# Performance work log

Hardware: AMD Instinct MI355X
Metric: run time of the kernel (lower is better)

## Reference

```python
import jax, jax.numpy as jnp
import numpy as np

N_EMBD = 768
N_EXP = 8
DIM_HIDDEN = int(N_EMBD * 4 * 2 / 3)  # 2048
B = 8
CAP = 1024


def setup_inputs() -> dict:
    key = jax.random.key(0)
    k1, k2, k3 = jax.random.split(key, 3)
    std_fc = N_EXP ** (-0.5)  # matches torch init: dim = c_fc.shape[0] = n_exp
    x = jax.random.normal(k1, (B, N_EXP, CAP, N_EMBD), dtype=jnp.float32)
    c_fc = jax.random.uniform(k2, (N_EXP, N_EMBD, 2 * DIM_HIDDEN), dtype=jnp.float32,
                              minval=-std_fc, maxval=std_fc)
    c_proj = jax.random.uniform(k3, (N_EXP, DIM_HIDDEN, N_EMBD), dtype=jnp.float32,
                                minval=-std_fc, maxval=std_fc)
    gamma = jnp.ones((N_EMBD,), dtype=jnp.float32)       # RMSNorm gamma
    mult_bias = jnp.ones((DIM_HIDDEN,), dtype=jnp.float32)  # GEGLU mult_bias
    return {"x": x, "c_fc": c_fc, "c_proj": c_proj, "gamma": gamma, "mult_bias": mult_bias}


def _moe_forward(x, c_fc, c_proj, gamma, mult_bias):
    # x: [b, e, n, d] -> [e, b, n, d]
    h = jnp.transpose(x, (1, 0, 2, 3))
    # RMSNorm (prenorm): F.normalize(x, dim=-1) * gamma * sqrt(d)
    scale = N_EMBD ** 0.5
    l2 = jnp.sqrt(jnp.sum(h * h, axis=-1, keepdims=True))
    h = h / jnp.maximum(l2, 1e-12) * gamma * scale
    # per-expert grouped GEMM: [e,b,n,d] @ [e,d,2h] -> [e,b,n,2h]
    u = jnp.einsum('ebnd,edh->ebnh', h, c_fc)
    # GEGLU: first half is value, second half is gate
    v, gate = u[..., :DIM_HIDDEN], u[..., DIM_HIDDEN:]
    g = jax.nn.gelu(gate, approximate=False) * v * mult_bias
    # project back: [e,b,n,h] @ [e,h,d] -> [e,b,n,d]
    out = jnp.einsum('ebnh,ehd->ebnd', g, c_proj)
    # back to [b, e, n, d]; dropout is identity (p=0.0)
    return jnp.transpose(out, (1, 0, 2, 3))


def reference(x, c_fc, c_proj, gamma, mult_bias):
    return _moe_forward(x, c_fc, c_proj, gamma, mult_bias)
```

## Files before the change

### kernel.cpp

```cpp
#include <hip/hip_runtime.h>
#include <math.h>

#define N_EMBD 768
#define N_EXP  8
#define DIMH   2048
#define CAPN   1024
#define M_TOT  8192

typedef __bf16 bf16x8 __attribute__((ext_vector_type(8)));
typedef float  f32x4  __attribute__((ext_vector_type(4)));

__device__ __forceinline__ unsigned short f2bf(float f) {
    unsigned int u = __float_as_uint(f);
    unsigned int r = (u + 0x7fffu + ((u >> 16) & 1u)) >> 16;
    return (unsigned short)r;
}

__device__ __forceinline__ void gload16(const void* g, void* l) {
    __builtin_amdgcn_global_load_lds(
        (const __attribute__((address_space(1))) unsigned int*)g,
        (__attribute__((address_space(3))) unsigned int*)l, 16, 0, 0);
}

__global__ __launch_bounds__(256) void norm_convert_kernel(
        const float* __restrict__ x, const float* __restrict__ gamma,
        unsigned short* __restrict__ h) {
    int r = blockIdx.x;
    int e = r >> 13, m = r & 8191;
    int b = m >> 10, nc = m & 1023;
    const float* row = x + (size_t)((b * N_EXP + e) * CAPN + nc) * N_EMBD;
    unsigned short* orow = h + (size_t)(e * M_TOT + m) * N_EMBD;
    int t = threadIdx.x;

    float v0 = row[t], v1 = row[t + 256], v2 = row[t + 512];
    float acc = v0 * v0 + v1 * v1 + v2 * v2;
#pragma unroll
    for (int off = 32; off >= 1; off >>= 1) acc += __shfl_down(acc, off, 64);
    __shared__ float part[4];
    if ((t & 63) == 0) part[t >> 6] = acc;
    __syncthreads();
    float tot = part[0] + part[1] + part[2] + part[3];
    float s = 27.712812921102035f / fmaxf(sqrtf(tot), 1e-12f);

    orow[t]       = f2bf(v0 * s * gamma[t]);
    orow[t + 256] = f2bf(v1 * s * gamma[t + 256]);
    orow[t + 512] = f2bf(v2 * s * gamma[t + 512]);
}

__global__ __launch_bounds__(256) void transpose_convert_kernel(
        const float* __restrict__ in, unsigned short* __restrict__ out, int R, int C) {
    __shared__ float tile[32][33];
    int c0 = blockIdx.x * 32, r0 = blockIdx.y * 32;
    const float* ip = in + (size_t)blockIdx.z * R * C;
    unsigned short* op = out + (size_t)blockIdx.z * R * C;
    int tx = threadIdx.x & 31, ty = threadIdx.x >> 5;
#pragma unroll
    for (int i = 0; i < 4; ++i)
        tile[ty + 8 * i][tx] = ip[(size_t)(r0 + ty + 8 * i) * C + c0 + tx];
    __syncthreads();
#pragma unroll
    for (int i = 0; i < 4; ++i)
        op[(size_t)(c0 + ty + 8 * i) * R + r0 + tx] = f2bf(tile[tx][ty + 8 * i]);
}

#define SBB  __builtin_amdgcn_s_barrier(); \
             asm volatile("s_waitcnt lgkmcnt(0)" ::: "memory"); \
             __builtin_amdgcn_sched_barrier(0); \
             __builtin_amdgcn_s_setprio(1)
#define SBE  __builtin_amdgcn_s_setprio(0); __builtin_amdgcn_s_barrier()
#define VMW(N) do { asm volatile("s_waitcnt vmcnt(" #N ")" ::: "memory"); \
             __builtin_amdgcn_sched_barrier(0); } while (0)

#define STG2(PSRC, RS, KT, DOFF) do { \
    gload16((PSRC) + (size_t)sr * (RS) + (size_t)(KT) * 64 + scs, lds + (DOFF) + ldst); \
    gload16((PSRC) + (size_t)(sr + 64) * (RS) + (size_t)(KT) * 64 + scs, lds + (DOFF) + ldst + 4096); \
  } while (0)

#define RDF(V) (*(const bf16x8*)(lds + (V)))

#define RDA4(AF, DB, IB) do { \
    _Pragma("unroll") for (int i_ = 0; i_ < 4; ++i_) { \
      AF[i_][0] = RDF((DB)*32768 + aB + ((IB) + i_)*1024 + sl0); \
      AF[i_][1] = RDF((DB)*32768 + aB + ((IB) + i_)*1024 + sl1); } \
  } while (0)

#define RDB2(BF, DB, BASE) do { \
    _Pragma("unroll") for (int j_ = 0; j_ < 2; ++j_) { \
      BF[j_][0] = RDF((DB)*32768 + (BASE) + j_*1024 + sl0); \
      BF[j_][1] = RDF((DB)*32768 + (BASE) + j_*1024 + sl1); } \
  } while (0)

#define QUAD(ACC, MS, NB, AF, BF) do { \
    _Pragma("unroll") for (int i_ = 0; i_ < 4; ++i_) \
    _Pragma("unroll") for (int j_ = 0; j_ < 2; ++j_) { \
      ACC[(MS)*4 + i_][(NB) + j_] = __builtin_amdgcn_mfma_f32_16x16x32_bf16( \
          AF[i_][0], BF[j_][0], ACC[(MS)*4 + i_][(NB) + j_], 0, 0, 0); \
      ACC[(MS)*4 + i_][(NB) + j_] = __builtin_amdgcn_mfma_f32_16x16x32_bf16( \
          AF[i_][1], BF[j_][1], ACC[(MS)*4 + i_][(NB) + j_], 0, 0, 0); } \
  } while (0)

__global__ __launch_bounds__(512, 2) void gemm1_kernel(
        const unsigned short* __restrict__ hb,
        const unsigned short* __restrict__ fT,
        const float* __restrict__ mbias,
        unsigned short* __restrict__ gb,
        int e0) {
    __shared__ __align__(16) unsigned short lds[65536];
    const int t = threadIdx.x;
    const int e = e0 + blockIdx.z;
    const int m0 = blockIdx.x * 256;
    const int n0 = blockIdx.y * 128;
    const unsigned short* pA  = hb + ((size_t)e * M_TOT + m0) * N_EMBD;
    const unsigned short* pBv = fT + ((size_t)e * 2 * DIMH + n0) * N_EMBD;
    const unsigned short* pBg = pBv + (size_t)DIMH * N_EMBD;
    unsigned short* pG = gb + (size_t)blockIdx.z * M_TOT * DIMH;

    const int sr   = t >> 3;
    const int scs  = ((t & 7) ^ (sr & 7)) * 8;
    const int ldst = t * 8;
    const int lane = t & 63, lo = lane & 15, quad = lane >> 4;
    const int w = t >> 6, wm = w & 1, wn = w >> 1;
    const int sl0 = ((quad    ) ^ (lo & 7)) * 8;
    const int sl1 = ((quad + 4) ^ (lo & 7)) * 8;
    const int aB  = wm * 8192 + lo * 64;
    const int bvB = 16384 + (wn * 32 + lo) * 64;
    const int bgB = 24576 + (wn * 32 + lo) * 64;

#define STA1(D, H, KT)  STG2(pA + (size_t)(H) * 128 * N_EMBD, N_EMBD, KT, (D)*32768 + (H)*8192)
#define STBV1(D, KT)    STG2(pBv, N_EMBD, KT, (D)*32768 + 16384)
#define STBG1(D, KT)    STG2(pBg, N_EMBD, KT, (D)*32768 + 24576)

    f32x4 accv[8][2], accg[8][2];
#pragma unroll
    for (int i = 0; i < 8; ++i)
#pragma unroll
        for (int j = 0; j < 2; ++j) { accv[i][j] = (f32x4)0.f; accg[i][j] = (f32x4)0.f; }
    bf16x8 a0[4][2], a1[4][2], bv[2][2], bg[2][2];

    STA1(0, 0, 0); STA1(0, 1, 0); STBV1(0, 0); STBG1(0, 0); STA1(1, 0, 1);
    VMW(2);
    __builtin_amdgcn_s_barrier();

    for (int it = 0; it < 6; ++it) {
        const int kb = 2 * it + 1, kc = kb + 1, kd = kb + 2;
        const bool more = (it < 5);
        RDA4(a0, 0, 0); RDB2(bv, 0, bvB);
        STA1(1, 1, kb);
        SBB; QUAD(accv, 0, 0, a0, bv); SBE;
        RDA4(a1, 0, 4);
        STBV1(1, kb);
        SBB; QUAD(accv, 1, 0, a1, bv); SBE;
        RDB2(bg, 0, bgB);
        STBG1(1, kb);
        SBB; QUAD(accg, 1, 0, a1, bg); SBE;
        if (more) { STA1(0, 0, kc); VMW(2); } else { VMW(0); }
        SBB; QUAD(accg, 0, 0, a0, bg); SBE;
        RDA4(a0, 1, 0); RDB2(bv, 1, bvB);
        if (more) STA1(0, 1, kc);
        SBB; QUAD(accv, 0, 0, a0, bv); SBE;
        RDA4(a1, 1, 4);
        if (more) STBV1(0, kc);
        SBB; QUAD(accv, 1, 0, a1, bv); SBE;
        RDB2(bg, 1, bgB);
        if (more) STBG1(0, kc);
        SBB; QUAD(accg, 1, 0, a1, bg); SBE;
        if (more) { STA1(1, 0, kd); VMW(2); } else { VMW(0); }
        SBB; QUAD(accg, 0, 0, a0, bg); SBE;
    }

#pragma unroll
    for (int i = 0; i < 8; ++i) {
        const int mb = m0 + wm * 128 + i * 16 + quad * 4;
#pragma unroll
        for (int j = 0; j < 2; ++j) {
            const int n = n0 + wn * 32 + j * 16 + lo;
            const float mbv = mbias[n];
#pragma unroll
            for (int r = 0; r < 4; ++r) {
                float gt = accg[i][j][r];
                float ge = 0.5f * gt * (1.0f + erff(gt * 0.70710678118654752f));
                pG[(size_t)(mb + r) * DIMH + n] = f2bf(ge * accv[i][j][r] * mbv);
            }
        }
    }
#undef STA1
#undef STBV1
#undef STBG1
}

__global__ __launch_bounds__(512, 2) void gemm2_kernel(
        const unsigned short* __restrict__ gb,
        const unsigned short* __restrict__ pT,
        float* __restrict__ out, int e0) {
    __shared__ __align__(16) unsigned short lds[65536];
    const int t = threadIdx.x;
    const int e = e0 + blockIdx.z;
    const int m0 = blockIdx.x * 256;
    const int n0 = blockIdx.y * 256;
    const unsigned short* pA = gb + (size_t)blockIdx.z * M_TOT * DIMH + (size_t)m0 * DIMH;
    const unsigned short* pB = pT + ((size_t)e * N_EMBD + n0) * DIMH;

    const int sr   = t >> 3;
    const int scs  = ((t & 7) ^ (sr & 7)) * 8;
    const int ldst = t * 8;
    const int lane = t & 63, lo = lane & 15, quad = lane >> 4;
    const int w = t >> 6, wm = w & 1, wn = w >> 1;
    const int sl0 = ((quad    ) ^ (lo & 7)) * 8;
    const int sl1 = ((quad + 4) ^ (lo & 7)) * 8;
    const int aB  = wm * 8192 + lo * 64;
    const int bB  = 16384 + (wn >> 1) * 8192 + ((wn & 1) * 64 + lo) * 64;

#define STA2(D, H, KT)  STG2(pA + (size_t)(H) * 128 * DIMH, DIMH, KT, (D)*32768 + (H)*8192)
#define STB2(D, H, KT)  STG2(pB + (size_t)(H) * 128 * DIMH, DIMH, KT, (D)*32768 + 16384 + (H)*8192)

    f32x4 acc[8][4];
#pragma unroll
    for (int i = 0; i < 8; ++i)
#pragma unroll
        for (int j = 0; j < 4; ++j) acc[i][j] = (f32x4)0.f;
    bf16x8 a0[4][2], a1[4][2], bb[2][2];

    STA2(0, 0, 0); STA2(0, 1, 0); STB2(0, 0, 0); STB2(0, 1, 0); STA2(1, 0, 1);
    VMW(2);
    __builtin_amdgcn_s_barrier();

    for (int it = 0; it < 16; ++it) {
        const int kb = 2 * it + 1, kc = kb + 1, kd = kb + 2;
        const bool more = (it < 15);
        RDA4(a0, 0, 0); RDB2(bb, 0, bB);
        STA2(1, 1, kb);
        SBB; QUAD(acc, 0, 0, a0, bb); SBE;
        RDA4(a1, 0, 4);
        STB2(1, 0, kb);
        SBB; QUAD(acc, 1, 0, a1, bb); SBE;
        RDB2(bb, 0, bB + 2048);
        STB2(1, 1, kb);
        SBB; QUAD(acc, 1, 2, a1, bb); SBE;
        if (more) { STA2(0, 0, kc); VMW(2); } else { VMW(0); }
        SBB; QUAD(acc, 0, 2, a0, bb); SBE;
        RDA4(a0, 1, 0); RDB2(bb, 1, bB);
        if (more) STA2(0, 1, kc);
        SBB; QUAD(acc, 0, 0, a0, bb); SBE;
        RDA4(a1, 1, 4);
        if (more) STB2(0, 0, kc);
        SBB; QUAD(acc, 1, 0, a1, bb); SBE;
        RDB2(bb, 1, bB + 2048);
        if (more) STB2(0, 1, kc);
        SBB; QUAD(acc, 1, 2, a1, bb); SBE;
        if (more) { STA2(1, 0, kd); VMW(2); } else { VMW(0); }
        SBB; QUAD(acc, 0, 2, a0, bb); SBE;
    }

#pragma unroll
    for (int i = 0; i < 8; ++i) {
        const int mb = m0 + wm * 128 + i * 16 + quad * 4;
#pragma unroll
        for (int r = 0; r < 4; ++r) {
            const int m = mb + r;
            const int b = m >> 10, nc = m & 1023;
            float* orow = out + (size_t)((b * N_EXP + e) * CAPN + nc) * N_EMBD;
#pragma unroll
            for (int j = 0; j < 4; ++j)
                orow[n0 + wn * 64 + j * 16 + lo] = acc[i][j][r];
        }
    }
#undef STA2
#undef STB2
}

extern "C" void kernel_launch(void* const* d_in, const int* in_sizes, int n_in,
                              void* d_out, int out_size, void* d_ws, size_t ws_size,
                              hipStream_t stream) {
    const float* x     = (const float*)d_in[0];
    const float* cfc   = (const float*)d_in[1];
    const float* cproj = (const float*)d_in[2];
    const float* gamma = (const float*)d_in[3];
    const float* mbias = (const float*)d_in[4];
    float* out = (float*)d_out;

    unsigned short* h      = (unsigned short*)d_ws;
    unsigned short* cfcT   = h + 50331648ull;
    unsigned short* cprojT = cfcT + 25165824ull;
    unsigned short* gbuf   = cprojT + 12582912ull;
    const size_t need_batched = 444596224ull;

    norm_convert_kernel<<<dim3(N_EXP * M_TOT), dim3(256), 0, stream>>>(x, gamma, h);
    transpose_convert_kernel<<<dim3(2 * DIMH / 32, N_EMBD / 32, N_EXP), dim3(256), 0, stream>>>(
        cfc, cfcT, N_EMBD, 2 * DIMH);
    transpose_convert_kernel<<<dim3(N_EMBD / 32, DIMH / 32, N_EXP), dim3(256), 0, stream>>>(
        cproj, cprojT, DIMH, N_EMBD);

    if (ws_size >= need_batched) {
        gemm1_kernel<<<dim3(M_TOT / 256, DIMH / 128, N_EXP), dim3(512), 0, stream>>>(
            h, cfcT, mbias, gbuf, 0);
        gemm2_kernel<<<dim3(M_TOT / 256, N_EMBD / 256, N_EXP), dim3(512), 0, stream>>>(
            gbuf, cprojT, out, 0);
    } else {
        for (int e = 0; e < N_EXP; ++e) {
            gemm1_kernel<<<dim3(M_TOT / 256, DIMH / 128, 1), dim3(512), 0, stream>>>(
                h, cfcT, mbias, gbuf, e);
            gemm2_kernel<<<dim3(M_TOT / 256, N_EMBD / 256, 1), dim3(512), 0, stream>>>(
                gbuf, cprojT, out, e);
        }
    }
}
```

Before: 1.263 ms.

## Restructure GEMM prefetch schedule, vectorize norm kernel, use polynomial erf GELU

The norm kernel now processes one row per wavefront with float4 loads, u16x4 stores and xor-shuffle reduction, which removes the shared-memory barrier and cuts the block count. Both GEMM kernels change their global-to-LDS prefetch: each half-iteration issues the whole next K tile at once, then waits with vmcnt(0) before the last MFMA quad, replacing the staggered issue with partial vmcnt waits. The GELU epilogue swaps erff for the Abramowitz-Stegun polynomial using a fast reciprocal and __expf. In exchange the GELU is slightly less accurate, and the coarser full waits may expose more load latency.

```diff
diff --git a/kernel.cpp b/kernel.cpp
--- a/kernel.cpp
+++ b/kernel.cpp
@@ -9,6 +9,7 @@
 
 typedef __bf16 bf16x8 __attribute__((ext_vector_type(8)));
 typedef float  f32x4  __attribute__((ext_vector_type(4)));
+typedef unsigned short u16x4 __attribute__((ext_vector_type(4)));
 
 __device__ __forceinline__ unsigned short f2bf(float f) {
     unsigned int u = __float_as_uint(f);
@@ -22,29 +23,47 @@
         (__attribute__((address_space(3))) unsigned int*)l, 16, 0, 0);
 }
 
+__device__ __forceinline__ float gelu_exact(float x) {
+    float ax = fabsf(x);
+    float z  = ax * 0.70710678118654752f;
+    float t  = __builtin_amdgcn_rcpf(fmaf(0.3275911f, z, 1.0f));
+    float p  = fmaf(t, 1.061405429f, -1.453152027f);
+    p = fmaf(p, t, 1.421413741f);
+    p = fmaf(p, t, -0.284496736f);
+    p = fmaf(p, t, 0.254829592f);
+    p = p * t;
+    float ez = __expf(-z * z);
+    float erfz = fmaf(-p, ez, 1.0f);
+    return 0.5f * fmaf(ax, erfz, x);
+}
+
 __global__ __launch_bounds__(256) void norm_convert_kernel(
         const float* __restrict__ x, const float* __restrict__ gamma,
         unsigned short* __restrict__ h) {
-    int r = blockIdx.x;
+    int r = (blockIdx.x << 2) | (threadIdx.x >> 6);
+    int lane = threadIdx.x & 63;
     int e = r >> 13, m = r & 8191;
     int b = m >> 10, nc = m & 1023;
-    const float* row = x + (size_t)((b * N_EXP + e) * CAPN + nc) * N_EMBD;
-    unsigned short* orow = h + (size_t)(e * M_TOT + m) * N_EMBD;
-    int t = threadIdx.x;
-
-    float v0 = row[t], v1 = row[t + 256], v2 = row[t + 512];
-    float acc = v0 * v0 + v1 * v1 + v2 * v2;
-#pragma unroll
-    for (int off = 32; off >= 1; off >>= 1) acc += __shfl_down(acc, off, 64);
-    __shared__ float part[4];
-    if ((t & 63) == 0) part[t >> 6] = acc;
-    __syncthreads();
-    float tot = part[0] + part[1] + part[2] + part[3];
-    float s = 27.712812921102035f / fmaxf(sqrtf(tot), 1e-12f);
-
-    orow[t]       = f2bf(v0 * s * gamma[t]);
-    orow[t + 256] = f2bf(v1 * s * gamma[t + 256]);
-    orow[t + 512] = f2bf(v2 * s * gamma[t + 512]);
+    const float4* row = (const float4*)(x + (size_t)((b * N_EXP + e) * CAPN + nc) * N_EMBD);
+    const float4* g4  = (const float4*)gamma;
+
+    float4 v0 = row[lane], v1 = row[lane + 64], v2 = row[lane + 128];
+    float acc = v0.x*v0.x + v0.y*v0.y + v0.z*v0.z + v0.w*v0.w
+              + v1.x*v1.x + v1.y*v1.y + v1.z*v1.z + v1.w*v1.w
+              + v2.x*v2.x + v2.y*v2.y + v2.z*v2.z + v2.w*v2.w;
+#pragma unroll
+    for (int off = 32; off >= 1; off >>= 1) acc += __shfl_xor(acc, off, 64);
+    float s = 27.712812921102035f / fmaxf(sqrtf(acc), 1e-12f);
+
+    float4 g0 = g4[lane], g1 = g4[lane + 64], g2 = g4[lane + 128];
+    u16x4* o4 = (u16x4*)(h + (size_t)(e * M_TOT + m) * N_EMBD);
+    u16x4 o;
+    o[0]=f2bf(v0.x*s*g0.x); o[1]=f2bf(v0.y*s*g0.y); o[2]=f2bf(v0.z*s*g0.z); o[3]=f2bf(v0.w*s*g0.w);
+    o4[lane] = o;
+    o[0]=f2bf(v1.x*s*g1.x); o[1]=f2bf(v1.y*s*g1.y); o[2]=f2bf(v1.z*s*g1.z); o[3]=f2bf(v1.w*s*g1.w);
+    o4[lane + 64] = o;
+    o[0]=f2bf(v2.x*s*g2.x); o[1]=f2bf(v2.y*s*g2.y); o[2]=f2bf(v2.z*s*g2.z); o[3]=f2bf(v2.w*s*g2.w);
+    o4[lane + 128] = o;
 }
 
 __global__ __launch_bounds__(256) void transpose_convert_kernel(
@@ -68,12 +87,12 @@
              __builtin_amdgcn_sched_barrier(0); \
              __builtin_amdgcn_s_setprio(1)
 #define SBE  __builtin_amdgcn_s_setprio(0); __builtin_amdgcn_s_barrier()
-#define VMW(N) do { asm volatile("s_waitcnt vmcnt(" #N ")" ::: "memory"); \
+#define VMW0 do { asm volatile("s_waitcnt vmcnt(0)" ::: "memory"); \
              __builtin_amdgcn_sched_barrier(0); } while (0)
 
-#define STG2(PSRC, RS, KT, DOFF) do { \
-    gload16((PSRC) + (size_t)sr * (RS) + (size_t)(KT) * 64 + scs, lds + (DOFF) + ldst); \
-    gload16((PSRC) + (size_t)(sr + 64) * (RS) + (size_t)(KT) * 64 + scs, lds + (DOFF) + ldst + 4096); \
+#define STG2(PSRC, RS, KO, DOFF) do { \
+    gload16((PSRC) + (size_t)sr * (RS) + (KO) + scs, lds + (DOFF) + ldst); \
+    gload16((PSRC) + (size_t)(sr + 64) * (RS) + (KO) + scs, lds + (DOFF) + ldst + 4096); \
   } while (0)
 
 #define RDF(V) (*(const bf16x8*)(lds + (V)))
@@ -126,9 +145,10 @@
     const int bvB = 16384 + (wn * 32 + lo) * 64;
     const int bgB = 24576 + (wn * 32 + lo) * 64;
 
-#define STA1(D, H, KT)  STG2(pA + (size_t)(H) * 128 * N_EMBD, N_EMBD, KT, (D)*32768 + (H)*8192)
-#define STBV1(D, KT)    STG2(pBv, N_EMBD, KT, (D)*32768 + 16384)
-#define STBG1(D, KT)    STG2(pBg, N_EMBD, KT, (D)*32768 + 24576)
+#define STA1(D, H, KO)  STG2(pA + (size_t)(H) * 128 * N_EMBD, N_EMBD, KO, (D)*32768 + (H)*8192)
+#define STBV1(D, KO)    STG2(pBv, N_EMBD, KO, (D)*32768 + 16384)
+#define STBG1(D, KO)    STG2(pBg, N_EMBD, KO, (D)*32768 + 24576)
+#define STALL1(D, KO)   do { STA1(D,0,KO); STA1(D,1,KO); STBV1(D,KO); STBG1(D,KO); } while (0)
 
     f32x4 accv[8][2], accg[8][2];
 #pragma unroll
@@ -137,35 +157,32 @@
         for (int j = 0; j < 2; ++j) { accv[i][j] = (f32x4)0.f; accg[i][j] = (f32x4)0.f; }
     bf16x8 a0[4][2], a1[4][2], bv[2][2], bg[2][2];
 
-    STA1(0, 0, 0); STA1(0, 1, 0); STBV1(0, 0); STBG1(0, 0); STA1(1, 0, 1);
-    VMW(2);
+    STALL1(0, 0);
+    VMW0;
     __builtin_amdgcn_s_barrier();
 
+    int ko = 64;
     for (int it = 0; it < 6; ++it) {
-        const int kb = 2 * it + 1, kc = kb + 1, kd = kb + 2;
         const bool more = (it < 5);
+        STALL1(1, ko);
         RDA4(a0, 0, 0); RDB2(bv, 0, bvB);
-        STA1(1, 1, kb);
         SBB; QUAD(accv, 0, 0, a0, bv); SBE;
         RDA4(a1, 0, 4);
-        STBV1(1, kb);
         SBB; QUAD(accv, 1, 0, a1, bv); SBE;
         RDB2(bg, 0, bgB);
-        STBG1(1, kb);
         SBB; QUAD(accg, 1, 0, a1, bg); SBE;
-        if (more) { STA1(0, 0, kc); VMW(2); } else { VMW(0); }
+        VMW0;
         SBB; QUAD(accg, 0, 0, a0, bg); SBE;
+        if (more) STALL1(0, ko + 64);
         RDA4(a0, 1, 0); RDB2(bv, 1, bvB);
-        if (more) STA1(0, 1, kc);
         SBB; QUAD(accv, 0, 0, a0, bv); SBE;
         RDA4(a1, 1, 4);
-        if (more) STBV1(0, kc);
         SBB; QUAD(accv, 1, 0, a1, bv); SBE;
         RDB2(bg, 1, bgB);
-        if (more) STBG1(0, kc);
         SBB; QUAD(accg, 1, 0, a1, bg); SBE;
-        if (more) { STA1(1, 0, kd); VMW(2); } else { VMW(0); }
+        VMW0;
         SBB; QUAD(accg, 0, 0, a0, bg); SBE;
+        ko += 128;
     }
 
 #pragma unroll
@@ -177,8 +194,7 @@
             const float mbv = mbias[n];
 #pragma unroll
             for (int r = 0; r < 4; ++r) {
-                float gt = accg[i][j][r];
-                float ge = 0.5f * gt * (1.0f + erff(gt * 0.70710678118654752f));
+                float ge = gelu_exact(accg[i][j][r]);
                 pG[(size_t)(mb + r) * DIMH + n] = f2bf(ge * accv[i][j][r] * mbv);
             }
         }
@@ -186,6 +202,7 @@
 #undef STA1
 #undef STBV1
 #undef STBG1
+#undef STALL1
 }
 
 __global__ __launch_bounds__(512, 2) void gemm2_kernel(
@@ -210,8 +227,9 @@
     const int aB  = wm * 8192 + lo * 64;
     const int bB  = 16384 + (wn >> 1) * 8192 + ((wn & 1) * 64 + lo) * 64;
 
-#define STA2(D, H, KT)  STG2(pA + (size_t)(H) * 128 * DIMH, DIMH, KT, (D)*32768 + (H)*8192)
-#define STB2(D, H, KT)  STG2(pB + (size_t)(H) * 128 * DIMH, DIMH, KT, (D)*32768 + 16384 + (H)*8192)
+#define STA2(D, H, KO)  STG2(pA + (size_t)(H) * 128 * DIMH, DIMH, KO, (D)*32768 + (H)*8192)
+#define STB2(D, H, KO)  STG2(pB + (size_t)(H) * 128 * DIMH, DIMH, KO, (D)*32768 + 16384 + (H)*8192)
+#define STALL2(D, KO)   do { STA2(D,0,KO); STA2(D,1,KO); STB2(D,0,KO); STB2(D,1,KO); } while (0)
 
     f32x4 acc[8][4];
 #pragma unroll
@@ -220,35 +238,32 @@
         for (int j = 0; j < 4; ++j) acc[i][j] = (f32x4)0.f;
     bf16x8 a0[4][2], a1[4][2], bb[2][2];
 
-    STA2(0, 0, 0); STA2(0, 1, 0); STB2(0, 0, 0); STB2(0, 1, 0); STA2(1, 0, 1);
-    VMW(2);
+    STALL2(0, 0);
+    VMW0;
     __builtin_amdgcn_s_barrier();
 
+    int ko = 64;
     for (int it = 0; it < 16; ++it) {
-        const int kb = 2 * it + 1, kc = kb + 1, kd = kb + 2;
         const bool more = (it < 15);
+        STALL2(1, ko);
         RDA4(a0, 0, 0); RDB2(bb, 0, bB);
-        STA2(1, 1, kb);
         SBB; QUAD(acc, 0, 0, a0, bb); SBE;
         RDA4(a1, 0, 4);
-        STB2(1, 0, kb);
         SBB; QUAD(acc, 1, 0, a1, bb); SBE;
         RDB2(bb, 0, bB + 2048);
-        STB2(1, 1, kb);
         SBB; QUAD(acc, 1, 2, a1, bb); SBE;
-        if (more) { STA2(0, 0, kc); VMW(2); } else { VMW(0); }
+        VMW0;
         SBB; QUAD(acc, 0, 2, a0, bb); SBE;
+        if (more) STALL2(0, ko + 64);
         RDA4(a0, 1, 0); RDB2(bb, 1, bB);
-        if (more) STA2(0, 1, kc);
         SBB; QUAD(acc, 0, 0, a0, bb); SBE;
         RDA4(a1, 1, 4);
-        if (more) STB2(0, 0, kc);
         SBB; QUAD(acc, 1, 0, a1, bb); SBE;
         RDB2(bb, 1, bB + 2048);
-        if (more) STB2(0, 1, kc);
         SBB; QUAD(acc, 1, 2, a1, bb); SBE;
-        if (more) { STA2(1, 0, kd); VMW(2); } else { VMW(0); }
+        VMW0;
         SBB; QUAD(acc, 0, 2, a0, bb); SBE;
+        ko += 128;
     }
 
 #pragma unroll
@@ -266,6 +281,7 @@
     }
 #undef STA2
 #undef STB2
+#undef STALL2
 }
 
 extern "C" void kernel_launch(void* const* d_in, const int* in_sizes, int n_in,
@@ -284,7 +300,7 @@
     unsigned short* gbuf   = cprojT + 12582912ull;
     const size_t need_batched = 444596224ull;
 
-    norm_convert_kernel<<<dim3(N_EXP * M_TOT), dim3(256), 0, stream>>>(x, gamma, h);
+    norm_convert_kernel<<<dim3(N_EXP * M_TOT / 4), dim3(256), 0, stream>>>(x, gamma, h);
     transpose_convert_kernel<<<dim3(2 * DIMH / 32, N_EMBD / 32, N_EXP), dim3(256), 0, stream>>>(
         cfc, cfcT, N_EMBD, 2 * DIMH);
     transpose_convert_kernel<<<dim3(N_EMBD / 32, DIMH / 32, N_EXP), dim3(256), 0, stream>>>(
```

New measurement: 1.196 ms. 1.06x faster.
